# Performance work log

Measured on AMD Instinct MI355X. Metric: run time of the kernel, lower is better.

## Reference

```python
import jax, jax.numpy as jnp
import numpy as np

B, S, D = 4, 2048, 1024
H, ADIM = 16, 64
HID = H * ADIM  # 1024


def setup_inputs() -> dict:
    key = jax.random.key(0)
    k1, k2, k3, k4 = jax.random.split(key, 4)
    iQ = jax.random.normal(k1, (B, S, D), dtype=jnp.float32)
    mask = jax.random.randint(k2, (B, S, S), 0, 2).astype(bool)
    Wa = jax.random.normal(k3, (3 * HID, D), dtype=jnp.float32) * (1.0 / np.sqrt(D))
    Wo = jax.random.normal(k4, (HID, HID), dtype=jnp.float32) * (1.0 / np.sqrt(HID))
    return {"iQ": iQ, "mask": mask, "Wa": Wa, "Wo": Wo}


def reference(iQ, mask, Wa, Wo):
    b, s, _ = iQ.shape
    # fused QKV projection: [B,S,3*HID]
    qkv = jnp.einsum("bsd,ed->bse", iQ, Wa)
    q, k, v = jnp.split(qkv, 3, axis=-1)
    # [B,S,HID] -> [B,H,S,ADIM]
    to_heads = lambda t: t.reshape(b, s, H, ADIM).transpose(0, 2, 1, 3)
    q, k, v = to_heads(q), to_heads(k), to_heads(v)
    scores = jnp.einsum("bhqd,bhkd->bhqk", q, k) / np.sqrt(ADIM).astype(np.float32)
    scores = jnp.where(mask[:, None, :, :], jnp.float32(-1e32), scores)
    attn = jax.nn.softmax(scores, axis=-1)
    o = jnp.einsum("bhqk,bhkd->bhqd", attn, v)
    o = o.transpose(0, 2, 1, 3).reshape(b, s, HID)
    return jnp.einsum("bse,oe->bso", o, Wo)
```

## Files before the change

kernel.cpp:

```cpp
#include <hip/hip_runtime.h>
#include <hip/hip_bf16.h>

typedef __bf16 bf16;
typedef __bf16 bfrag __attribute__((ext_vector_type(8)));
typedef __bf16 bf16x2 __attribute__((ext_vector_type(2)));
typedef float f32x4 __attribute__((ext_vector_type(4)));
typedef float f32x16 __attribute__((ext_vector_type(16)));
typedef unsigned u32x2 __attribute__((ext_vector_type(2)));

constexpr int Bc = 4, Sc = 2048, Hc = 16, ADc = 64, HIDc = 1024;
constexpr size_t QKV_ELEMS = (size_t)Bc * Hc * Sc * ADc;

__device__ __forceinline__ void gload_lds16(const void* g, void* lds) {
  __builtin_amdgcn_global_load_lds(
      (const __attribute__((address_space(1))) unsigned int*)g,
      (__attribute__((address_space(3))) unsigned int*)lds, 16, 0, 0);
}

__device__ __forceinline__ bfrag ldb(const bf16* p) {
  return *(const bfrag*)p;
}

__device__ __forceinline__ unsigned pack2(float lo, float hi) {
  union { bf16x2 h; unsigned u; } c;
  c.h = bf16x2{(bf16)lo, (bf16)hi};
  return c.u;
}

__device__ __forceinline__ void plswap(unsigned& a, unsigned& b) {
  u32x2 r = __builtin_amdgcn_permlane32_swap(a, b, false, false);
  a = r.x;
  b = r.y;
}

__device__ __forceinline__ f32x16 zero16() {
  f32x16 z;
#pragma unroll
  for (int i = 0; i < 16; ++i) z[i] = 0.f;
  return z;
}

__global__ __launch_bounds__(256) void f2b3(const float* __restrict__ s0,
                                            const float* __restrict__ s1,
                                            const float* __restrict__ s2,
                                            bf16* __restrict__ d0,
                                            bf16* __restrict__ d1,
                                            bf16* __restrict__ d2) {
  const int blk = blockIdx.x;
  const float* s;
  bf16* d;
  size_t base;
  if (blk < 4096)      { s = s0; d = d0; base = (size_t)blk * 2048; }
  else if (blk < 5632) { s = s1; d = d1; base = (size_t)(blk - 4096) * 2048; }
  else                 { s = s2; d = d2; base = (size_t)(blk - 5632) * 2048; }
  const size_t i = base + (size_t)threadIdx.x * 8;
  const float4 a = *(const float4*)(s + i);
  const float4 b = *(const float4*)(s + i + 4);
  bfrag o = {(bf16)a.x, (bf16)a.y, (bf16)a.z, (bf16)a.w,
             (bf16)b.x, (bf16)b.y, (bf16)b.z, (bf16)b.w};
  *(bfrag*)(d + i) = o;
}

template <int MODE>
__global__ __launch_bounds__(256) void gemm_bt(
    const bf16* __restrict__ A,
    const bf16* __restrict__ Bm,
    bf16* __restrict__ C0,
    bf16* __restrict__ C1,
    bf16* __restrict__ C2,
    float* __restrict__ Cf,
    int Kdim, int Ndim)
{
  __shared__ __align__(16) bf16 As[128 * 32];
  __shared__ __align__(16) bf16 Bs[128 * 32];

  const int tid  = threadIdx.x;
  const int wave = tid >> 6;
  const int lane = tid & 63;
  const int n16  = lane & 15;
  const int quad = lane >> 4;
  const int wm   = wave & 1;
  const int wn   = wave >> 1;
  const int m0   = blockIdx.y * 128;
  const int n0   = blockIdx.x * 128;

  const f32x4 fzero = {0.f, 0.f, 0.f, 0.f};
  f32x4 acc[4][4];
#pragma unroll
  for (int i = 0; i < 4; ++i)
#pragma unroll
    for (int j = 0; j < 4; ++j) acc[i][j] = fzero;

  const int lcol = (lane & 3) * 8;

  for (int k0 = 0; k0 < Kdim; k0 += 32) {
#pragma unroll
    for (int c = 0; c < 2; ++c) {
      const int chunk = wave * 2 + c;
      const int row   = chunk * 16 + (lane >> 2);
      const bf16* agp;
      if (MODE == 0) {
        agp = A + (size_t)(m0 + row) * Kdim + k0 + lcol;
      } else {
        const int gs = m0 + row;
        const int h  = k0 >> 6;
        agp = A + (((size_t)(gs >> 11) * Hc + h) * Sc + (gs & 2047)) * ADc
                + (k0 & 63) + lcol;
      }
      gload_lds16(agp, (char*)As + chunk * 1024);
      gload_lds16(Bm + (size_t)(n0 + row) * Kdim + k0 + lcol,
                  (char*)Bs + chunk * 1024);
    }
    __syncthreads();

    bfrag af[4], bf[4];
#pragma unroll
    for (int i = 0; i < 4; ++i)
      af[i] = ldb(As + (wm * 64 + i * 16 + n16) * 32 + quad * 8);
#pragma unroll
    for (int j = 0; j < 4; ++j)
      bf[j] = ldb(Bs + (wn * 64 + j * 16 + n16) * 32 + quad * 8);
#pragma unroll
    for (int i = 0; i < 4; ++i)
#pragma unroll
      for (int j = 0; j < 4; ++j)
        acc[i][j] = __builtin_amdgcn_mfma_f32_16x16x32_bf16(af[i], bf[j], acc[i][j], 0, 0, 0);
    __syncthreads();
  }

#pragma unroll
  for (int i = 0; i < 4; ++i) {
    const int grow = m0 + wm * 64 + i * 16 + quad * 4;
#pragma unroll
    for (int j = 0; j < 4; ++j) {
      const int col_local = wn * 64 + j * 16 + n16;
#pragma unroll
      for (int r = 0; r < 4; ++r) {
        const int row = grow + r;
        const float v = acc[i][j][r];
        if (MODE == 1) {
          Cf[(size_t)row * Ndim + n0 + col_local] = v;
        } else {
          const int seg = n0 >> 10;
          const int hid = (n0 & 1023) + col_local;
          const int h = hid >> 6, a = hid & 63;
          const int bi = row >> 11, s = row & 2047;
          if (seg == 0)
            C0[(((size_t)bi * Hc + h) * Sc + s) * ADc + a] = (bf16)(v * 0.125f);
          else if (seg == 1)
            C1[(((size_t)bi * Hc + h) * Sc + s) * ADc + a] = (bf16)v;
          else
            C2[(((size_t)bi * Hc + h) * ADc + a) * Sc + s] = (bf16)v;
        }
      }
    }
  }
}

__global__ __launch_bounds__(256) void mask_pack(const int* __restrict__ mask,
                                                 unsigned* __restrict__ bits) {
  const int w = blockIdx.x * 256 + threadIdx.x;
  const int4* p = (const int4*)(mask + (size_t)w * 32);
  unsigned out = 0;
#pragma unroll
  for (int i = 0; i < 8; ++i) {
    int4 m = p[i];
    out |= (unsigned)(m.x != 0) << (i * 4);
    out |= (unsigned)(m.y != 0) << (i * 4 + 1);
    out |= (unsigned)(m.z != 0) << (i * 4 + 2);
    out |= (unsigned)(m.w != 0) << (i * 4 + 3);
  }
  bits[w] = out;
}

__global__ __launch_bounds__(512, 4) void attn(
    const bf16* __restrict__ Qw,
    const bf16* __restrict__ Kw,
    const bf16* __restrict__ Vtw,
    const unsigned* __restrict__ mbits,
    bf16* __restrict__ Ow)
{
  __shared__ __align__(16) bf16 Ks[2][64 * 64];
  __shared__ __align__(16) bf16 Vs[2][64 * 64];

  const int tid  = threadIdx.x;
  const int wave = tid >> 6, lane = tid & 63;
  const int l31  = lane & 31, hi = lane >> 5;
  const int sw   = lane & 7;
  const int bh   = blockIdx.x >> 3, qb = blockIdx.x & 7;
  const int b    = bh >> 4;
  const int q0w  = qb * 256 + wave * 32;

  const int srow = tid >> 3;
  const int scol = (tid & 7) * 8;
  const bf16* gK = Kw  + ((size_t)bh * Sc + srow) * ADc + scol;
  const bf16* gV = Vtw + ((size_t)bh * ADc + srow) * Sc + scol;
  const int soff = srow * 64 + (scol ^ ((srow & 7) * 8));

  const bf16* qrow = Qw + ((size_t)bh * Sc + q0w + l31) * ADc + hi * 8;
  bfrag qf[4];
#pragma unroll
  for (int ks = 0; ks < 4; ++ks) qf[ks] = ldb(qrow + ks * 16);

  f32x16 of0 = zero16();
  f32x16 of1 = zero16();
  float li = 0.f;

  const unsigned* mq = mbits + ((size_t)b * Sc + q0w + l31) * (Sc / 32);

  auto tile_compute = [&](const bf16* Kbuf, const bf16* Vbuf, unsigned mx,
                          unsigned my) {
#pragma unroll
    for (int nt = 0; nt < 2; ++nt) {
      f32x16 sf = zero16();
#pragma unroll
      for (int ks = 0; ks < 4; ++ks) {
        const bfrag kf = ldb(Kbuf + (nt * 32 + l31) * 64 + (((2 * ks + hi) ^ sw) * 8));
        sf = __builtin_amdgcn_mfma_f32_32x32x16_bf16(kf, qf[ks], sf, 0, 0, 0);
      }

      const unsigned w = (nt ? my : mx) >> (hi * 4);
      unsigned D[8];
#pragma unroll
      for (int m = 0; m < 8; ++m) {
        const int r0 = 2 * m, r1 = r0 + 1;
        float p0 = __expf(sf[r0]);
        float p1 = __expf(sf[r1]);
        if ((w >> ((r0 & 3) + 8 * (r0 >> 2))) & 1u) p0 = 0.f;
        if ((w >> ((r1 & 3) + 8 * (r1 >> 2))) & 1u) p1 = 0.f;
        li += p0 + p1;
        D[m] = pack2(p0, p1);
      }

#pragma unroll
      for (int a = 0; a < 2; ++a) {
        unsigned w0 = D[4 * a + 0], w2 = D[4 * a + 2];
        plswap(w0, w2);
        unsigned w1 = D[4 * a + 1], w3 = D[4 * a + 3];
        plswap(w1, w3);
        union { unsigned u[4]; bfrag f; } pu;
        pu.u[0] = w0; pu.u[1] = w1; pu.u[2] = w2; pu.u[3] = w3;
        const int vg = ((4 * nt + 2 * a + hi) ^ sw) * 8;
        const bfrag vf0 = ldb(Vbuf + l31 * 64 + vg);
        of0 = __builtin_amdgcn_mfma_f32_32x32x16_bf16(pu.f, vf0, of0, 0, 0, 0);
        const bfrag vf1 = ldb(Vbuf + (32 + l31) * 64 + vg);
        of1 = __builtin_amdgcn_mfma_f32_32x32x16_bf16(pu.f, vf1, of1, 0, 0, 0);
      }
    }
  };

  {
    const bfrag k0 = ldb(gK);
    const bfrag v0 = ldb(gV);
    const bfrag k1 = ldb(gK + (size_t)64 * ADc);
    const bfrag v1 = ldb(gV + 64);
    *(bfrag*)(Ks[0] + soff) = k0;
    *(bfrag*)(Vs[0] + soff) = v0;
    *(bfrag*)(Ks[1] + soff) = k1;
    *(bfrag*)(Vs[1] + soff) = v1;
  }
  __syncthreads();

  for (int kt = 0; kt < Sc / 64; kt += 2) {
    const int kn = (kt + 2) & 31;
    const bfrag kp0 = ldb(gK + (size_t)kn * 64 * ADc);
    const bfrag vp0 = ldb(gV + kn * 64);
    const bfrag kp1 = ldb(gK + (size_t)(kn + 1) * 64 * ADc);
    const bfrag vp1 = ldb(gV + (kn + 1) * 64);

    const uint4 mwv = *(const uint4*)(mq + kt * 2);

    tile_compute(Ks[0], Vs[0], mwv.x, mwv.y);
    tile_compute(Ks[1], Vs[1], mwv.z, mwv.w);

    __syncthreads();
    *(bfrag*)(Ks[0] + soff) = kp0;
    *(bfrag*)(Vs[0] + soff) = vp0;
    *(bfrag*)(Ks[1] + soff) = kp1;
    *(bfrag*)(Vs[1] + soff) = vp1;
    __syncthreads();
  }

  const float s = li + __shfl_xor(li, 32);
  const float inv = 1.f / s;
#pragma unroll
  for (int r = 0; r < 16; ++r) {
    const int query = (r & 3) + 8 * (r >> 2) + 4 * hi;
    const float invr = __shfl(inv, query);
    bf16* orow = Ow + ((size_t)bh * Sc + q0w + query) * ADc + l31;
    orow[0]  = (bf16)(of0[r] * invr);
    orow[32] = (bf16)(of1[r] * invr);
  }
}

extern "C" void kernel_launch(void* const* d_in, const int* in_sizes, int n_in,
                              void* d_out, int out_size, void* d_ws, size_t ws_size,
                              hipStream_t stream) {
  const float* iQ = (const float*)d_in[0];
  const int* mask = (const int*)d_in[1];
  const float* Wa = (const float*)d_in[2];
  const float* Wo = (const float*)d_in[3];
  float* out      = (float*)d_out;

  bf16* iQb       = (bf16*)d_out;
  bf16* Wab       = iQb + QKV_ELEMS;
  unsigned* mbits = (unsigned*)(Wab + 3145728);
  bf16* Qw  = (bf16*)d_ws;
  bf16* Kw  = Qw + QKV_ELEMS;
  bf16* Vtw = Kw + QKV_ELEMS;
  bf16* Wob = Vtw + QKV_ELEMS;

  f2b3<<<dim3(6144), 256, 0, stream>>>(iQ, Wa, Wo, iQb, Wab, Wob);
  mask_pack<<<dim3((Bc * Sc * Sc / 32) / 256), 256, 0, stream>>>(mask, mbits);
  gemm_bt<0><<<dim3(24, 64), 256, 0, stream>>>(iQb, Wab, Qw, Kw, Vtw, nullptr, 1024, 3072);
  attn<<<dim3(Bc * Hc * 8), 512, 0, stream>>>(Qw, Kw, Vtw, mbits, Qw);
  gemm_bt<1><<<dim3(8, 64), 256, 0, stream>>>(Qw, Wob, nullptr, nullptr, nullptr, out, 1024, 1024);
}
```

Measured before the change: 390.2 us.

## Stage K/V tiles via direct global-to-LDS loads with single-tile double buffering

Replaces the register-staged K/V loads with global_load_lds direct-to-LDS copies and restructures the loop from two tiles per iteration with two barriers into a ping-pong double buffer that prefetches the next tile during compute and uses one barrier per iteration. The aim is to cut VGPR pressure and LDS write instructions and to overlap memory with MFMA work. The cost is twice as many loop iterations and barriers per tile. The swizzle moves from the LDS address to the global address, and correctness depends on the wave-uniform LDS destination layout matching the XOR-swizzled reads.

```diff
diff --git a/kernel.cpp b/kernel.cpp
--- a/kernel.cpp
+++ b/kernel.cpp
@@ -191,11 +191,11 @@
   const int b    = bh >> 4;
   const int q0w  = qb * 256 + wave * 32;
 
-  const int srow = tid >> 3;
-  const int scol = (tid & 7) * 8;
-  const bf16* gK = Kw  + ((size_t)bh * Sc + srow) * ADc + scol;
-  const bf16* gV = Vtw + ((size_t)bh * ADc + srow) * Sc + scol;
-  const int soff = srow * 64 + (scol ^ ((srow & 7) * 8));
+  const int drow = wave * 8 + (lane >> 3);
+  const int dchk = ((lane & 7) ^ (lane >> 3)) * 8;
+  const bf16* gK = Kw  + ((size_t)bh * Sc + drow) * ADc + dchk;
+  const bf16* gV = Vtw + ((size_t)bh * ADc + drow) * Sc + dchk;
+  const int ldsb = wave * 1024;
 
   const bf16* qrow = Qw + ((size_t)bh * Sc + q0w + l31) * ADc + hi * 8;
   bfrag qf[4];
@@ -249,35 +249,21 @@
     }
   };
 
-  {
-    const bfrag k0 = ldb(gK);
-    const bfrag v0 = ldb(gV);
-    const bfrag k1 = ldb(gK + (size_t)64 * ADc);
-    const bfrag v1 = ldb(gV + 64);
-    *(bfrag*)(Ks[0] + soff) = k0;
-    *(bfrag*)(Vs[0] + soff) = v0;
-    *(bfrag*)(Ks[1] + soff) = k1;
-    *(bfrag*)(Vs[1] + soff) = v1;
-  }
+  auto stage = [&](int buf, int kt) {
+    gload_lds16(gK + (size_t)kt * 64 * ADc, (char*)Ks[buf] + ldsb);
+    gload_lds16(gV + (size_t)kt * 64,       (char*)Vs[buf] + ldsb);
+  };
+
+  stage(0, 0);
   __syncthreads();
 
-  for (int kt = 0; kt < Sc / 64; kt += 2) {
-    const int kn = (kt + 2) & 31;
-    const bfrag kp0 = ldb(gK + (size_t)kn * 64 * ADc);
-    const bfrag vp0 = ldb(gV + kn * 64);
-    const bfrag kp1 = ldb(gK + (size_t)(kn + 1) * 64 * ADc);
-    const bfrag vp1 = ldb(gV + (kn + 1) * 64);
-
-    const uint4 mwv = *(const uint4*)(mq + kt * 2);
-
-    tile_compute(Ks[0], Vs[0], mwv.x, mwv.y);
-    tile_compute(Ks[1], Vs[1], mwv.z, mwv.w);
-
-    __syncthreads();
-    *(bfrag*)(Ks[0] + soff) = kp0;
-    *(bfrag*)(Vs[0] + soff) = vp0;
-    *(bfrag*)(Ks[1] + soff) = kp1;
-    *(bfrag*)(Vs[1] + soff) = vp1;
+  for (int kt = 0; kt < Sc / 64; ++kt) {
+    const int cur = kt & 1;
+    if (kt + 1 < Sc / 64) stage(cur ^ 1, kt + 1);
+
+    const uint2 mwv = *(const uint2*)(mq + kt * 2);
+    tile_compute(Ks[cur], Vs[cur], mwv.x, mwv.y);
+
     __syncthreads();
   }
 
```

Result: faster. 380.1 us (-2.6%).
